# Performance work log

Hardware: AMD Instinct MI355X
Metric: run time of the kernel (lower is better)

## Reference

```python
import jax, jax.numpy as jnp
import numpy as np

NUM_HEADS = 8


def setup_inputs() -> dict:
    key = jax.random.key(0)
    ks = jax.random.split(key, 8)
    B, N, H, W = 8, 1024, 32, 32
    dim = H * W  # 1024
    x1 = jax.random.normal(ks[0], (B, N, H, W), dtype=jnp.float32)
    x2 = jax.random.normal(ks[1], (B, N, H, W), dtype=jnp.float32)
    conv_w = jax.random.normal(ks[2], (N, 2 * N, 3, 3), dtype=jnp.float32) * 0.01
    conv_b = jnp.zeros((N,), dtype=jnp.float32)
    wq = jax.random.normal(ks[3], (dim, dim), dtype=jnp.float32) * 0.02
    wk = jax.random.normal(ks[4], (dim, dim), dtype=jnp.float32) * 0.02
    wv = jax.random.normal(ks[5], (dim, dim), dtype=jnp.float32) * 0.02
    proj_w = jax.random.normal(ks[6], (dim, dim), dtype=jnp.float32) * 0.02
    proj_b = jnp.zeros((dim,), dtype=jnp.float32)
    return {"x1": x1, "x2": x2, "conv_w": conv_w, "conv_b": conv_b,
            "wq": wq, "wk": wk, "wv": wv, "proj_w": proj_w, "proj_b": proj_b}


def reference(x1, x2, conv_w, conv_b, wq, wk, wv, proj_w, proj_b):
    B, N, H, W = x1.shape
    C = H * W
    nh = NUM_HEADS
    hd = C // nh
    scale = hd ** -0.5

    # conv_cat: Conv2d(2N -> N, k=3, pad=1) on channel-concatenated inputs
    x_cat = jnp.concatenate([x1, x2], axis=1)  # [B, 2N, H, W]
    x_cat = jax.lax.conv_general_dilated(
        x_cat, conv_w, window_strides=(1, 1), padding=((1, 1), (1, 1)),
        dimension_numbers=("NCHW", "OIHW", "NCHW"))
    x_cat = x_cat + conv_b[None, :, None, None]
    x_cat = x_cat.reshape(B, N, C)  # [B, N, C]

    # torch Linear: y = x @ W.T (no bias, qkv_bias=False)
    def heads(t):  # [B, N, C] -> [B, nh, N, hd]
        return t.reshape(B, N, nh, hd).transpose(0, 2, 1, 3)

    q = heads(x1.reshape(B, N, C) @ wq.T)
    k = heads(x_cat @ wk.T)
    v = heads(x_cat @ wv.T)

    # attention: softmax(q k^T * scale) v   (dropout is identity at p=0)
    attn = jnp.einsum("bhnd,bhmd->bhnm", q, k) * scale
    attn = jax.nn.softmax(attn, axis=-1)
    x_attn = jnp.einsum("bhnm,bhmd->bhnd", attn, v)  # [B, nh, N, hd]
    x_attn = x_attn.transpose(0, 2, 1, 3).reshape(B, N, C)

    out = (x_attn @ proj_w.T + proj_b).reshape(B, N, H, W) + x1
    return out
```

## Files before the change

kernel.cpp:

```cpp
#include <hip/hip_runtime.h>
#include <hip/hip_bf16.h>
#include <cstdint>
#include <cstddef>

typedef __attribute__((ext_vector_type(8))) short short8;
typedef __attribute__((ext_vector_type(4))) float f32x4;
typedef unsigned short u16;

static __device__ __forceinline__ u16 f2bf(float f) {
  __hip_bfloat16 h = __float2bfloat16(f);
  return *reinterpret_cast<u16*>(&h);
}

static __device__ __forceinline__ void gload16(const void* g, void* l) {
  __builtin_amdgcn_global_load_lds(
      (const __attribute__((address_space(1))) void*)g,
      (__attribute__((address_space(3))) void*)l, 16, 0, 0);
}


__global__ void cast4_k(const float* __restrict__ a, const float* __restrict__ b,
                        const float* __restrict__ c, const float* __restrict__ d,
                        u16* __restrict__ oa, u16* __restrict__ ob,
                        u16* __restrict__ oc, u16* __restrict__ od) {
  const int which = blockIdx.y;
  const float* src = (which == 0) ? a : (which == 1) ? b : (which == 2) ? c : d;
  u16* dst = (which == 0) ? oa : (which == 1) ? ob : (which == 2) ? oc : od;
  int i = blockIdx.x * 256 + threadIdx.x;
  float4 v = ((const float4*)src)[i];
  union { u16 u[4]; uint2 p; } r;
  r.u[0] = f2bf(v.x); r.u[1] = f2bf(v.y); r.u[2] = f2bf(v.z); r.u[3] = f2bf(v.w);
  ((uint2*)dst)[i] = r.p;
}

__global__ void build_pad(const float* __restrict__ x1, const float* __restrict__ x2,
                          u16* __restrict__ in_t_pad, u16* __restrict__ x1b) {
  __shared__ float tile[64][65];
  const int it = blockIdx.x;
  const int st = blockIdx.y;
  const int b  = blockIdx.z;
  const int i0 = it * 64, s0 = st * 64;
  const bool isx1 = (i0 < 1024);
  const float* src = isx1
      ? x1 + ((size_t)b * 1024 + i0) * 1024
      : x2 + ((size_t)b * 1024 + (i0 - 1024)) * 1024;
  const int t = threadIdx.x;
  #pragma unroll
  for (int jj = 0; jj < 16; ++jj) {
    int idx = jj * 256 + t;
    int ii = idx >> 6, si = idx & 63;
    float v = src[(size_t)ii * 1024 + s0 + si];
    tile[ii][si] = v;
    if (isx1)
      x1b[((size_t)b * 1024 + i0 + ii) * 1024 + s0 + si] = f2bf(v);
  }
  __syncthreads();
  #pragma unroll
  for (int jj = 0; jj < 16; ++jj) {
    int idx = jj * 256 + t;
    int si = idx >> 6, ii = idx & 63;
    const int s = s0 + si;
    const int prow = (b * 34 + (s >> 5) + 1) * 34 + (s & 31) + 1;
    in_t_pad[(size_t)prow * 2048 + i0 + ii] = f2bf(tile[ii][si]);
  }
}

__global__ void pack_wp(const float* __restrict__ cw, u16* __restrict__ Wp) {
  __shared__ float sb[2304];
  const int blk = blockIdx.x;
  const int t = threadIdx.x;
  const size_t base = (size_t)blk * 2304;
  #pragma unroll
  for (int jj = 0; jj < 9; ++jj) sb[jj * 256 + t] = cw[base + jj * 256 + t];
  __syncthreads();
  const int p = blk * 256 + t;
  #pragma unroll
  for (int q = 0; q < 9; ++q)
    Wp[(size_t)q * 2097152 + p] = f2bf(sb[t * 9 + q]);
}

__global__ void addc_k(const float* __restrict__ p, const float* __restrict__ bias,
                       u16* __restrict__ xc) {
  __shared__ float tile[64][65];
  const int st = blockIdx.x;
  const int ot = blockIdx.y;
  const int b  = blockIdx.z;
  const int s0 = st * 64, o0 = ot * 64;
  const int t = threadIdx.x;
  const float* p1 = p + 8388608;
  #pragma unroll
  for (int jj = 0; jj < 16; ++jj) {
    int idx = jj * 256 + t;
    int si = idx >> 6, oi = idx & 63;
    const size_t m = ((size_t)b * 1024 + s0 + si) * 1024 + o0 + oi;
    tile[si][oi] = p[m] + p1[m] + bias[o0 + oi];
  }
  __syncthreads();
  #pragma unroll
  for (int jj = 0; jj < 16; ++jj) {
    int idx = jj * 256 + t;
    int oi = idx >> 6, si = idx & 63;
    xc[((size_t)b * 1024 + o0 + oi) * 1024 + s0 + si] = f2bf(tile[si][oi]);
  }
}

enum { GM_PLAIN = 0, GM_PROJ = 2, GM_KV = 4 };

__global__ __launch_bounds__(256, 1)
void conv9_k(const u16* __restrict__ Ap, const u16* __restrict__ B,
             float* __restrict__ Cf) {
  __shared__ u16 lds[2 * 12288 + 3 * 8192];
  const int tid = threadIdx.x;
  const int lane = tid & 63, w = tid >> 6;
  const int l15 = lane & 15, l4 = lane >> 4;

  const int bid = blockIdx.x;
  const int lb = (bid & 7) * 32 + (bid >> 3);
  const int kz = lb >> 7;
  const int tile = lb & 127;
  const int tm = tile >> 2, tn = tile & 3;
  const int row0 = tm * 256, col0 = tn * 256;
  const int b = tm >> 2;
  const int y0 = (tm & 3) * 8;
  const int hb = (b * 34 + y0) * 34;
  const int wr = (w >> 1) * 128, wc = (w & 1) * 128;
  const int chbase = kz * 1024;

  int pr[8];
  #pragma unroll
  for (int mi = 0; mi < 8; ++mi) {
    const int m = row0 + wr + mi * 16 + l15;
    const int y = (m >> 5) & 31, x = m & 31;
    pr[mi] = (y - y0 + 1) * 34 + x + 1;
  }

  const int srow = tid >> 2;
  const int sgc = tid & 3;

  f32x4 acc[8][8];
  #pragma unroll
  for (int i = 0; i < 8; ++i)
    #pragma unroll
    for (int jj = 0; jj < 8; ++jj)
      acc[i][jj] = (f32x4){0.f, 0.f, 0.f, 0.f};

  auto stageHalo = [&](int cc, int half) {
    u16* dst = lds + half * 12288;
    #pragma unroll
    for (int rnd = 0; rnd < 6; ++rnd) {
      const int row = rnd * 64 + srow;
      const int g = sgc ^ ((row >> 1) & 3);
      const u16* src = Ap + (size_t)(hb + row) * 2048 + chbase + cc * 32 + g * 8;
      gload16(src, dst + (size_t)(rnd * 256 + tid) * 8);
    }
  };
  auto stageB = [&](int cc, int q) {
    u16* dst = lds + 24576 + (q % 3) * 8192;
    #pragma unroll
    for (int rnd = 0; rnd < 4; ++rnd) {
      const int r = rnd * 64 + srow;
      const int g = sgc ^ ((r >> 1) & 3);
      const u16* src = B + ((size_t)q << 21) + (size_t)(col0 + r) * 2048
                       + chbase + cc * 32 + g * 8;
      gload16(src, dst + (size_t)(rnd * 256 + tid) * 8);
    }
  };

  constexpr int ddt[9] = {-35, -34, -33, -1, 0, 1, 33, 34, 35};
  constexpr int NC = 32;

  stageHalo(0, 0);
  stageHalo(1, 1);
  stageB(0, 0);
  stageB(0, 1);

  for (int cc = 0; cc < NC; ++cc) {
    const u16* hcur = lds + (cc & 1) * 12288;
    const bool interior = (cc >= 1 && cc <= NC - 2);
    #pragma unroll
    for (int q = 0; q < 9; ++q) {
      if ((q == 1 || q == 2) && interior) {
        asm volatile("s_waitcnt vmcnt(10)" ::: "memory");
      } else if (q == 8 && cc == NC - 1) {
        asm volatile("s_waitcnt vmcnt(0)" ::: "memory");
      } else {
        asm volatile("s_waitcnt vmcnt(4)" ::: "memory");
      }
      __builtin_amdgcn_s_barrier();
      {
        const int gp2 = cc * 9 + q + 2;
        if (gp2 <= NC * 9 - 1) {
          int qS = q + 2, ccS = cc;
          if (qS >= 9) { qS -= 9; ccS += 1; }
          stageB(ccS, qS);
        }
        if (q == 0 && cc >= 1 && cc <= NC - 2)
          stageHalo(cc + 1, (cc + 1) & 1);
      }
      {
        const u16* bq = lds + 24576 + (q % 3) * 8192;
        const int dd = ddt[q];
        short8 av[8], bv[8];
        #pragma unroll
        for (int mi = 0; mi < 8; ++mi) {
          const int hr = pr[mi] + dd;
          const int g = l4 ^ ((hr >> 1) & 3);
          av[mi] = *(const short8*)(hcur + hr * 32 + g * 8);
        }
        #pragma unroll
        for (int ni = 0; ni < 8; ++ni) {
          const int r = wc + ni * 16 + l15;
          const int g = l4 ^ ((r >> 1) & 3);
          bv[ni] = *(const short8*)(bq + r * 32 + g * 8);
        }
        __builtin_amdgcn_s_setprio(1);
        #pragma unroll
        for (int mi = 0; mi < 8; ++mi)
          #pragma unroll
          for (int ni = 0; ni < 8; ++ni)
            acc[mi][ni] = __builtin_amdgcn_mfma_f32_16x16x32_bf16(av[mi], bv[ni], acc[mi][ni], 0, 0, 0);
        __builtin_amdgcn_s_setprio(0);
      }
    }
  }

  #pragma unroll
  for (int mi = 0; mi < 8; ++mi) {
    #pragma unroll
    for (int ni = 0; ni < 8; ++ni) {
      #pragma unroll
      for (int j = 0; j < 4; ++j) {
        const int grow = row0 + wr + mi * 16 + l4 * 4 + j;
        const int gcol = col0 + wc + ni * 16 + l15;
        Cf[(size_t)kz * 8388608 + ((size_t)grow << 10) + gcol] = acc[mi][ni][j];
      }
    }
  }
}

template<int MODE>
__global__ __launch_bounds__(512, 2)
void gemm3_k(const u16* __restrict__ A, const u16* __restrict__ B,
             u16* __restrict__ Cb, float* __restrict__ Cf,
             const float* __restrict__ bias, const float* __restrict__ resid,
             int Ktot, int ntn_sh) {
  __shared__ u16 lds[3 * 24576];
  const int tid = threadIdx.x;
  const int lane = tid & 63;
  const int w = tid >> 6;
  const int l15 = lane & 15, l4 = lane >> 4;

  const int nwg = gridDim.x;
  const int bid = blockIdx.x;
  const int lb = (bid & 7) * (nwg >> 3) + (bid >> 3);
  const int tm = lb >> ntn_sh;
  const int tn = lb & ((1 << ntn_sh) - 1);
  const int row0 = tm * 256, col0 = tn * 128;
  const int wr = (w >> 1) * 64, wc = (w & 1) * 64;

  const int sr = w * 8 + (lane >> 3);
  const int pp = (lane & 7) ^ (lane >> 3);

  f32x4 acc[4][4];
  #pragma unroll
  for (int i = 0; i < 4; ++i)
    #pragma unroll
    for (int jj = 0; jj < 4; ++jj)
      acc[i][jj] = (f32x4){0.f, 0.f, 0.f, 0.f};

  const int nK = Ktot >> 6;

  auto stage = [&](int kt, u16* buf) {
    u16* da = buf + (size_t)w * 512;
    u16* db = buf + 16384 + (size_t)w * 512;
    const int k0 = kt << 6;
    #pragma unroll
    for (int u = 0; u < 4; ++u) {
      const u16* ga = A + (size_t)(row0 + u * 64 + sr) * Ktot + k0 + pp * 8;
      gload16(ga, da + u * 4096);
    }
    #pragma unroll
    for (int u = 0; u < 2; ++u) {
      const u16* gb = B + (size_t)(col0 + u * 64 + sr) * Ktot + k0 + pp * 8;
      gload16(gb, db + u * 4096);
    }
  };

  auto compute = [&](const u16* buf) {
    const char* Ar = (const char*)buf;
    const char* Br = (const char*)(buf + 16384);
    #pragma unroll
    for (int ks = 0; ks < 2; ++ks) {
      const int bcol = ((ks << 6) + (l4 << 4)) ^ ((l15 & 7) << 4);
      short8 av[4], bv[4];
      #pragma unroll
      for (int mi = 0; mi < 4; ++mi)
        av[mi] = *(const short8*)(Ar + (wr + mi * 16 + l15) * 128 + bcol);
      #pragma unroll
      for (int ni = 0; ni < 4; ++ni)
        bv[ni] = *(const short8*)(Br + (wc + ni * 16 + l15) * 128 + bcol);
      __builtin_amdgcn_s_setprio(1);
      #pragma unroll
      for (int mi = 0; mi < 4; ++mi)
        #pragma unroll
        for (int ni = 0; ni < 4; ++ni)
          acc[mi][ni] = __builtin_amdgcn_mfma_f32_16x16x32_bf16(av[mi], bv[ni], acc[mi][ni], 0, 0, 0);
      __builtin_amdgcn_s_setprio(0);
    }
  };

  u16* pb0 = lds;
  u16* pb1 = lds + 24576;
  u16* pb2 = lds + 49152;

  stage(0, pb0);
  stage(1, pb1);
  for (int t = 0; t < nK; ++t) {
    if (t + 1 < nK) {
      asm volatile("s_waitcnt vmcnt(6)" ::: "memory");
    } else {
      asm volatile("s_waitcnt vmcnt(0)" ::: "memory");
    }
    __builtin_amdgcn_s_barrier();
    if (t + 2 < nK) stage(t + 2, pb2);
    compute(pb0);
    u16* tmp = pb0; pb0 = pb1; pb1 = pb2; pb2 = tmp;
  }

  #pragma unroll
  for (int mi = 0; mi < 4; ++mi) {
    #pragma unroll
    for (int ni = 0; ni < 4; ++ni) {
      #pragma unroll
      for (int j = 0; j < 4; ++j) {
        const int grow = row0 + wr + mi * 16 + l4 * 4 + j;
        const int gcol = col0 + wc + ni * 16 + l15;
        const float v = acc[mi][ni][j];
        if constexpr (MODE == GM_PLAIN) {
          Cb[((size_t)grow << 10) + gcol] = f2bf(v);
        } else if constexpr (MODE == GM_PROJ) {
          const size_t o = ((size_t)grow << 10) + gcol;
          Cf[o] = v + bias[gcol] + resid[o];
        }
      }
    }
  }
}

template<int MODE>
__global__ __launch_bounds__(512, 4)
void gemm5_k(const u16* __restrict__ A, const u16* __restrict__ B,
             u16* __restrict__ Cb, u16* __restrict__ Cb2,
             int Ktot, int ntn_sh) {
  __shared__ u16 lds[3 * 12288];
  const int tid = threadIdx.x;
  const int lane = tid & 63;
  const int w = tid >> 6;
  const int l15 = lane & 15, l4 = lane >> 4;

  const int nwg = gridDim.x;
  const int bid = blockIdx.x;
  const int lb = (bid & 7) * (nwg >> 3) + (bid >> 3);
  const int tm = lb >> ntn_sh;
  const int tn = lb & ((1 << ntn_sh) - 1);
  const int row0 = tm * 256, col0 = tn * 128;
  const int wr = (w >> 1) * 64, wc = (w & 1) * 64;

  const int str = tid >> 2;
  const int sgc = tid & 3;

  f32x4 acc[4][4];
  #pragma unroll
  for (int i = 0; i < 4; ++i)
    #pragma unroll
    for (int jj = 0; jj < 4; ++jj)
      acc[i][jj] = (f32x4){0.f, 0.f, 0.f, 0.f};

  const int nKt = Ktot >> 5;

  auto stage = [&](int kt, u16* buf) {
    const int k0 = kt << 5;
    #pragma unroll
    for (int u = 0; u < 2; ++u) {
      const int r = u * 128 + str;
      const int swz = sgc ^ ((r >> 1) & 3);
      const u16* ga = A + (size_t)(row0 + r) * Ktot + k0 + swz * 8;
      gload16(ga, buf + ((size_t)u * 512 + tid) * 8);
    }
    {
      const int swz = sgc ^ ((str >> 1) & 3);
      const u16* gb = B + (size_t)(col0 + str) * Ktot + k0 + swz * 8;
      gload16(gb, buf + 8192 + (size_t)tid * 8);
    }
  };

  auto compute = [&](const u16* buf) {
    short8 av[4], bv[4];
    #pragma unroll
    for (int mi = 0; mi < 4; ++mi) {
      const int row = wr + mi * 16 + l15;
      const int g = l4 ^ ((row >> 1) & 3);
      av[mi] = *(const short8*)(buf + row * 32 + g * 8);
    }
    #pragma unroll
    for (int ni = 0; ni < 4; ++ni) {
      const int row = wc + ni * 16 + l15;
      const int g = l4 ^ ((row >> 1) & 3);
      bv[ni] = *(const short8*)(buf + 8192 + row * 32 + g * 8);
    }
    __builtin_amdgcn_s_setprio(1);
    #pragma unroll
    for (int mi = 0; mi < 4; ++mi)
      #pragma unroll
      for (int ni = 0; ni < 4; ++ni)
        acc[mi][ni] = __builtin_amdgcn_mfma_f32_16x16x32_bf16(av[mi], bv[ni], acc[mi][ni], 0, 0, 0);
    __builtin_amdgcn_s_setprio(0);
  };

  u16* pb0 = lds;
  u16* pb1 = lds + 12288;
  u16* pb2 = lds + 24576;

  stage(0, pb0);
  stage(1, pb1);
  for (int t = 0; t < nKt; ++t) {
    if (t + 1 < nKt) {
      asm volatile("s_waitcnt vmcnt(3)" ::: "memory");
    } else {
      asm volatile("s_waitcnt vmcnt(0)" ::: "memory");
    }
    __builtin_amdgcn_s_barrier();
    if (t + 2 < nKt) stage(t + 2, pb2);
    compute(pb0);
    u16* tmp = pb0; pb0 = pb1; pb1 = pb2; pb2 = tmp;
  }

  if constexpr (MODE == GM_KV) {
    if (col0 < 1024) {
      #pragma unroll
      for (int mi = 0; mi < 4; ++mi)
        #pragma unroll
        for (int ni = 0; ni < 4; ++ni)
          #pragma unroll
          for (int j = 0; j < 4; ++j) {
            const int grow = row0 + wr + mi * 16 + l4 * 4 + j;
            const int gcol = col0 + wc + ni * 16 + l15;
            Cb[((size_t)grow << 10) + gcol] = f2bf(acc[mi][ni][j]);
          }
    } else {
      const int h = (col0 - 1024) >> 7;
      const int bb = row0 >> 10;
      u16* tb = lds;
      #pragma unroll
      for (int chunk = 0; chunk < 4; ++chunk) {
        __syncthreads();
        if ((w >> 1) == chunk) {
          #pragma unroll
          for (int mi = 0; mi < 4; ++mi)
            #pragma unroll
            for (int ni = 0; ni < 4; ++ni)
              #pragma unroll
              for (int j = 0; j < 4; ++j) {
                const int d = wc + ni * 16 + l15;
                const int t = mi * 16 + l4 * 4 + j;
                tb[d * 66 + t] = f2bf(acc[mi][ni][j]);
              }
        }
        __syncthreads();
        {
          const int r = tid >> 2;
          const int c0 = (tid & 3) * 16;
          const int tok = (row0 & 1023) + chunk * 64 + c0;
          uint4 v0 = *(const uint4*)(tb + r * 66 + c0);
          uint4 v1 = *(const uint4*)(tb + r * 66 + c0 + 8);
          u16* dst = Cb2 + (((size_t)((bb * 8 + h) * 128 + r)) << 10) + tok;
          *(uint4*)dst = v0;
          *(uint4*)(dst + 8) = v1;
        }
      }
    }
  }
}

__global__ __launch_bounds__(256, 2)
void attn2_k(const u16* __restrict__ Q, const u16* __restrict__ K,
             const u16* __restrict__ Vt, u16* __restrict__ O) {
  __shared__ u16 Ks[2][64 * 128];
  __shared__ u16 Vs[2][128 * 64];
  __shared__ u16 Plds[4][16 * 80];
  const int bid = blockIdx.x;
  const int lb = (bid & 7) * 128 + (bid >> 3);
  const int bh = lb >> 4;
  const int mtile = lb & 15;
  const int b = bh >> 3, h = bh & 7;
  const int tid = threadIdx.x, lane = tid & 63, w = tid >> 6;
  const int l15 = lane & 15, l4 = lane >> 4;

  short8 qf[4];
  {
    const int qrow = b * 1024 + mtile * 64 + w * 16 + l15;
    const u16* qb = Q + ((size_t)qrow << 10) + h * 128;
    #pragma unroll
    for (int kk = 0; kk < 4; ++kk)
      qf[kk] = *(const short8*)(qb + kk * 32 + l4 * 8);
  }

  f32x4 o[8];
  #pragma unroll
  for (int db = 0; db < 8; ++db) o[db] = (f32x4){0.f, 0.f, 0.f, 0.f};
  float mrow[4], lrow[4];
  #pragma unroll
  for (int j = 0; j < 4; ++j) { mrow[j] = -1e30f; lrow[j] = 0.f; }
  const float scale = 0.08838834764831845f;

  auto stageKV = [&](int kt, int half) {
    #pragma unroll
    for (int j = 0; j < 4; ++j) {
      const int c = (j * 4 + w) * 64 + lane;
      const int r = c >> 4;
      const int coff = (((c & 15) ^ (r & 7)) << 3);
      const u16* gp = K + ((size_t)(b * 1024 + kt * 64 + r) << 10) + h * 128 + coff;
      gload16(gp, (void*)(Ks[half] + (j * 4 + w) * 512));
    }
    #pragma unroll
    for (int j = 0; j < 4; ++j) {
      const int c = (j * 4 + w) * 64 + lane;
      const int r = c >> 3;
      const int coff = (((c & 7) ^ (r & 7)) << 3);
      const u16* gp = Vt + ((size_t)((b * 8 + h) * 128 + r) << 10) + kt * 64 + coff;
      gload16(gp, (void*)(Vs[half] + (j * 4 + w) * 512));
    }
  };

  stageKV(0, 0);
  for (int kt = 0; kt < 16; ++kt) {
    const int cur = kt & 1;
    asm volatile("s_waitcnt vmcnt(0)" ::: "memory");
    __builtin_amdgcn_s_barrier();
    if (kt + 1 < 16) stageKV(kt + 1, cur ^ 1);

    const u16* ks_ = Ks[cur];
    const u16* vs_ = Vs[cur];
    f32x4 s[4];
    #pragma unroll
    for (int cb = 0; cb < 4; ++cb) {
      s[cb] = (f32x4){0.f, 0.f, 0.f, 0.f};
      #pragma unroll
      for (int kk = 0; kk < 4; ++kk) {
        const int col = (kk * 32 + l4 * 8) ^ ((l15 & 7) << 3);
        short8 bK = *(const short8*)(ks_ + (cb * 16 + l15) * 128 + col);
        s[cb] = __builtin_amdgcn_mfma_f32_16x16x32_bf16(qf[kk], bK, s[cb], 0, 0, 0);
      }
    }
    #pragma unroll
    for (int cb = 0; cb < 4; ++cb) {
      s[cb][0] *= scale; s[cb][1] *= scale; s[cb][2] *= scale; s[cb][3] *= scale;
    }
    #pragma unroll
    for (int j = 0; j < 4; ++j) {
      float mx = fmaxf(fmaxf(s[0][j], s[1][j]), fmaxf(s[2][j], s[3][j]));
      #pragma unroll
      for (int off = 8; off >= 1; off >>= 1)
        mx = fmaxf(mx, __shfl_xor(mx, off, 64));
      const float mn = fmaxf(mrow[j], mx);
      const float fac = __expf(mrow[j] - mn);
      mrow[j] = mn;
      float rs = 0.f;
      #pragma unroll
      for (int cb = 0; cb < 4; ++cb) {
        const float p = __expf(s[cb][j] - mn);
        s[cb][j] = p;
        rs += p;
      }
      #pragma unroll
      for (int off = 8; off >= 1; off >>= 1)
        rs += __shfl_xor(rs, off, 64);
      lrow[j] = lrow[j] * fac + rs;
      #pragma unroll
      for (int db = 0; db < 8; ++db) o[db][j] *= fac;
    }
    u16* pl = Plds[w];
    #pragma unroll
    for (int cb = 0; cb < 4; ++cb)
      #pragma unroll
      for (int j = 0; j < 4; ++j)
        pl[(l4 * 4 + j) * 80 + cb * 16 + l15] = f2bf(s[cb][j]);
    asm volatile("s_waitcnt lgkmcnt(0)" ::: "memory");
    __builtin_amdgcn_sched_barrier(0);
    short8 ap[2];
    #pragma unroll
    for (int ks2 = 0; ks2 < 2; ++ks2)
      ap[ks2] = *(const short8*)(pl + l15 * 80 + ks2 * 32 + l4 * 8);
    #pragma unroll
    for (int db = 0; db < 8; ++db) {
      #pragma unroll
      for (int ks2 = 0; ks2 < 2; ++ks2) {
        const int col = (ks2 * 32 + l4 * 8) ^ ((l15 & 7) << 3);
        short8 bV = *(const short8*)(vs_ + (db * 16 + l15) * 64 + col);
        o[db] = __builtin_amdgcn_mfma_f32_16x16x32_bf16(ap[ks2], bV, o[db], 0, 0, 0);
      }
    }
  }
  #pragma unroll
  for (int db = 0; db < 8; ++db) {
    #pragma unroll
    for (int j = 0; j < 4; ++j) {
      const int grow = b * 1024 + mtile * 64 + w * 16 + l4 * 4 + j;
      const int gcol = h * 128 + db * 16 + l15;
      O[((size_t)grow << 10) + gcol] = f2bf(o[db][j] / lrow[j]);
    }
  }
}


extern "C" void kernel_launch(void* const* d_in, const int* in_sizes, int n_in,
                              void* d_out, int out_size, void* d_ws, size_t ws_size,
                              hipStream_t stream) {
  const float* x1     = (const float*)d_in[0];
  const float* x2     = (const float*)d_in[1];
  const float* conv_w = (const float*)d_in[2];
  const float* conv_b = (const float*)d_in[3];
  const float* wq     = (const float*)d_in[4];
  const float* wk     = (const float*)d_in[5];
  const float* wv     = (const float*)d_in[6];
  const float* proj_w = (const float*)d_in[7];
  const float* proj_b = (const float*)d_in[8];
  float* out = (float*)d_out;

  char* ws = (char*)d_ws;
  size_t off = 0;
  auto alloc = [&](size_t bytes) -> void* {
    void* p = ws + off;
    off += (bytes + 255) & ~(size_t)255;
    return p;
  };
  u16* x1b  = (u16*)alloc(8192ULL * 1024 * 2);
  u16* in_t_pad = (u16*)alloc((9248ULL + 96) * 2048 * 2);
  const size_t pad_bytes = 9248ULL * 2048 * 2;
  u16* Wp   = (u16*)alloc(9ULL * 2097152 * 2);
  u16* wqb  = (u16*)alloc(1048576ULL * 2);
  u16* wkb  = (u16*)alloc(1048576ULL * 2);
  u16* wvb  = (u16*)alloc(1048576ULL * 2);
  u16* pjb  = (u16*)alloc(1048576ULL * 2);
  u16* xc   = (u16*)alloc(8192ULL * 1024 * 2);
  u16* Qb   = (u16*)alloc(8192ULL * 1024 * 2);
  u16* Kb   = (u16*)alloc(8192ULL * 1024 * 2);
  u16* Vtb  = (u16*)alloc(8192ULL * 1024 * 2);
  u16* Ob   = (u16*)alloc(8192ULL * 1024 * 2);
  float* pConv = (float*)Qb;

  (void)hipMemsetAsync(in_t_pad, 0, pad_bytes + 96ULL * 2048 * 2, stream);
  cast4_k<<<dim3(1024, 4), 256, 0, stream>>>(wq, wk, wv, proj_w, wqb, wkb, wvb, pjb);
  build_pad<<<dim3(32, 16, 8), 256, 0, stream>>>(x1, x2, in_t_pad, x1b);
  pack_wp<<<8192, 256, 0, stream>>>(conv_w, Wp);

  conv9_k<<<256, 256, 0, stream>>>(in_t_pad, Wp, pConv);
  addc_k<<<dim3(16, 16, 8), 256, 0, stream>>>(pConv, conv_b, xc);
  gemm3_k<GM_PLAIN><<<256, 512, 0, stream>>>(x1b, wqb, Qb, nullptr, nullptr, nullptr, 1024, 3);
  gemm5_k<GM_KV><<<512, 512, 0, stream>>>(xc, wkb, Kb, Vtb, 1024, 4);
  attn2_k<<<1024, 256, 0, stream>>>(Qb, Kb, Vtb, Ob);
  gemm3_k<GM_PROJ><<<256, 512, 0, stream>>>(Ob, pjb, nullptr, out, proj_b, x1, 1024, 3);
}
```

Baseline: 495.5 us.

## Merge Q/K/V GEMMs into one launch, prefetch conv A fragments, tweak attention

Measured after the change: 551.8 us. +11.4%, slower.

```diff
diff --git a/kernel.cpp b/kernel.cpp
--- a/kernel.cpp
+++ b/kernel.cpp
@@ -104,11 +104,11 @@
   }
 }
 
-enum { GM_PLAIN = 0, GM_PROJ = 2, GM_KV = 4 };
+enum { GM_PLAIN = 0, GM_PROJ = 2 };
 
 __global__ __launch_bounds__(256, 1)
-void conv9_k(const u16* __restrict__ Ap, const u16* __restrict__ B,
-             float* __restrict__ Cf) {
+void conv11_k(const u16* __restrict__ Ap, const u16* __restrict__ B,
+              float* __restrict__ Cf) {
   __shared__ u16 lds[2 * 12288 + 3 * 8192];
   const int tid = threadIdx.x;
   const int lane = tid & 63, w = tid >> 6;
@@ -174,6 +174,8 @@
   stageB(0, 0);
   stageB(0, 1);
 
+  short8 avb[2][8];
+
   for (int cc = 0; cc < NC; ++cc) {
     const u16* hcur = lds + (cc & 1) * 12288;
     const bool interior = (cc >= 1 && cc <= NC - 2);
@@ -199,26 +201,35 @@
       }
       {
         const u16* bq = lds + 24576 + (q % 3) * 8192;
-        const int dd = ddt[q];
-        short8 av[8], bv[8];
-        #pragma unroll
-        for (int mi = 0; mi < 8; ++mi) {
-          const int hr = pr[mi] + dd;
-          const int g = l4 ^ ((hr >> 1) & 3);
-          av[mi] = *(const short8*)(hcur + hr * 32 + g * 8);
+        if (q == 0) {
+          #pragma unroll
+          for (int mi = 0; mi < 8; ++mi) {
+            const int hr = pr[mi] + ddt[0];
+            const int g = l4 ^ ((hr >> 1) & 3);
+            avb[0][mi] = *(const short8*)(hcur + hr * 32 + g * 8);
+          }
         }
+        short8 bv[8];
         #pragma unroll
         for (int ni = 0; ni < 8; ++ni) {
           const int r = wc + ni * 16 + l15;
           const int g = l4 ^ ((r >> 1) & 3);
           bv[ni] = *(const short8*)(bq + r * 32 + g * 8);
         }
+        if (q < 8) {
+          #pragma unroll
+          for (int mi = 0; mi < 8; ++mi) {
+            const int hr = pr[mi] + ddt[q + 1];
+            const int g = l4 ^ ((hr >> 1) & 3);
+            avb[(q + 1) & 1][mi] = *(const short8*)(hcur + hr * 32 + g * 8);
+          }
+        }
         __builtin_amdgcn_s_setprio(1);
         #pragma unroll
         for (int mi = 0; mi < 8; ++mi)
           #pragma unroll
           for (int ni = 0; ni < 8; ++ni)
-            acc[mi][ni] = __builtin_amdgcn_mfma_f32_16x16x32_bf16(av[mi], bv[ni], acc[mi][ni], 0, 0, 0);
+            acc[mi][ni] = __builtin_amdgcn_mfma_f32_16x16x32_bf16(avb[q & 1][mi], bv[ni], acc[mi][ni], 0, 0, 0);
         __builtin_amdgcn_s_setprio(0);
       }
     }
@@ -347,25 +358,28 @@
   }
 }
 
-template<int MODE>
 __global__ __launch_bounds__(512, 4)
-void gemm5_k(const u16* __restrict__ A, const u16* __restrict__ B,
-             u16* __restrict__ Cb, u16* __restrict__ Cb2,
-             int Ktot, int ntn_sh) {
+void qkv_k(const u16* __restrict__ Ax1, const u16* __restrict__ Axc,
+           const u16* __restrict__ Wq, const u16* __restrict__ Wk,
+           const u16* __restrict__ Wv,
+           u16* __restrict__ Qb, u16* __restrict__ Kb, u16* __restrict__ Vtb) {
   __shared__ u16 lds[3 * 12288];
   const int tid = threadIdx.x;
   const int lane = tid & 63;
   const int w = tid >> 6;
   const int l15 = lane & 15, l4 = lane >> 4;
 
-  const int nwg = gridDim.x;
   const int bid = blockIdx.x;
-  const int lb = (bid & 7) * (nwg >> 3) + (bid >> 3);
-  const int tm = lb >> ntn_sh;
-  const int tn = lb & ((1 << ntn_sh) - 1);
+  const int lb = (bid & 7) * 96 + (bid >> 3);
+  const int sel = lb >> 8;
+  const int sub = lb & 255;
+  const int tm = sub >> 3, tn = sub & 7;
   const int row0 = tm * 256, col0 = tn * 128;
   const int wr = (w >> 1) * 64, wc = (w & 1) * 64;
 
+  const u16* A = (sel == 0) ? Ax1 : Axc;
+  const u16* B = (sel == 0) ? Wq : (sel == 1) ? Wk : Wv;
+
   const int str = tid >> 2;
   const int sgc = tid & 3;
 
@@ -376,6 +390,7 @@
     for (int jj = 0; jj < 4; ++jj)
       acc[i][jj] = (f32x4){0.f, 0.f, 0.f, 0.f};
 
+  constexpr int Ktot = 1024;
   const int nKt = Ktot >> 5;
 
   auto stage = [&](int kt, u16* buf) {
@@ -435,48 +450,47 @@
     u16* tmp = pb0; pb0 = pb1; pb1 = pb2; pb2 = tmp;
   }
 
-  if constexpr (MODE == GM_KV) {
-    if (col0 < 1024) {
-      #pragma unroll
-      for (int mi = 0; mi < 4; ++mi)
+  if (sel < 2) {
+    u16* Cb = (sel == 0) ? Qb : Kb;
+    #pragma unroll
+    for (int mi = 0; mi < 4; ++mi)
+      #pragma unroll
+      for (int ni = 0; ni < 4; ++ni)
         #pragma unroll
-        for (int ni = 0; ni < 4; ++ni)
+        for (int j = 0; j < 4; ++j) {
+          const int grow = row0 + wr + mi * 16 + l4 * 4 + j;
+          const int gcol = col0 + wc + ni * 16 + l15;
+          Cb[((size_t)grow << 10) + gcol] = f2bf(acc[mi][ni][j]);
+        }
+  } else {
+    const int h = tn;
+    const int bb = row0 >> 10;
+    u16* tb = lds;
+    #pragma unroll
+    for (int chunk = 0; chunk < 4; ++chunk) {
+      __syncthreads();
+      if ((w >> 1) == chunk) {
+        #pragma unroll
+        for (int mi = 0; mi < 4; ++mi)
           #pragma unroll
-          for (int j = 0; j < 4; ++j) {
-            const int grow = row0 + wr + mi * 16 + l4 * 4 + j;
-            const int gcol = col0 + wc + ni * 16 + l15;
-            Cb[((size_t)grow << 10) + gcol] = f2bf(acc[mi][ni][j]);
-          }
-    } else {
-      const int h = (col0 - 1024) >> 7;
-      const int bb = row0 >> 10;
-      u16* tb = lds;
-      #pragma unroll
-      for (int chunk = 0; chunk < 4; ++chunk) {
-        __syncthreads();
-        if ((w >> 1) == chunk) {
-          #pragma unroll
-          for (int mi = 0; mi < 4; ++mi)
+          for (int ni = 0; ni < 4; ++ni)
             #pragma unroll
-            for (int ni = 0; ni < 4; ++ni)
-              #pragma unroll
-              for (int j = 0; j < 4; ++j) {
-                const int d = wc + ni * 16 + l15;
-                const int t = mi * 16 + l4 * 4 + j;
-                tb[d * 66 + t] = f2bf(acc[mi][ni][j]);
-              }
-        }
-        __syncthreads();
-        {
-          const int r = tid >> 2;
-          const int c0 = (tid & 3) * 16;
-          const int tok = (row0 & 1023) + chunk * 64 + c0;
-          uint4 v0 = *(const uint4*)(tb + r * 66 + c0);
-          uint4 v1 = *(const uint4*)(tb + r * 66 + c0 + 8);
-          u16* dst = Cb2 + (((size_t)((bb * 8 + h) * 128 + r)) << 10) + tok;
-          *(uint4*)dst = v0;
-          *(uint4*)(dst + 8) = v1;
-        }
+            for (int j = 0; j < 4; ++j) {
+              const int d = wc + ni * 16 + l15;
+              const int t = mi * 16 + l4 * 4 + j;
+              tb[d * 66 + t] = f2bf(acc[mi][ni][j]);
+            }
+      }
+      __syncthreads();
+      {
+        const int r = tid >> 2;
+        const int c0 = (tid & 3) * 16;
+        const int tok = (row0 & 1023) + chunk * 64 + c0;
+        uint4 v0 = *(const uint4*)(tb + r * 66 + c0);
+        uint4 v1 = *(const uint4*)(tb + r * 66 + c0 + 8);
+        u16* dst = Vtb + (((size_t)((bb * 8 + h) * 128 + r)) << 10) + tok;
+        *(uint4*)dst = v0;
+        *(uint4*)(dst + 8) = v1;
       }
     }
   }
@@ -487,7 +501,7 @@
              const u16* __restrict__ Vt, u16* __restrict__ O) {
   __shared__ u16 Ks[2][64 * 128];
   __shared__ u16 Vs[2][128 * 64];
-  __shared__ u16 Plds[4][16 * 80];
+  __shared__ u16 Plds[4][16 * 72];
   const int bid = blockIdx.x;
   const int lb = (bid & 7) * 128 + (bid >> 3);
   const int bh = lb >> 4;
@@ -549,7 +563,9 @@
       for (int kk = 0; kk < 4; ++kk) {
         const int col = (kk * 32 + l4 * 8) ^ ((l15 & 7) << 3);
         short8 bK = *(const short8*)(ks_ + (cb * 16 + l15) * 128 + col);
+        __builtin_amdgcn_s_setprio(1);
         s[cb] = __builtin_amdgcn_mfma_f32_16x16x32_bf16(qf[kk], bK, s[cb], 0, 0, 0);
+        __builtin_amdgcn_s_setprio(0);
       }
     }
     #pragma unroll
@@ -584,20 +600,22 @@
     for (int cb = 0; cb < 4; ++cb)
       #pragma unroll
       for (int j = 0; j < 4; ++j)
-        pl[(l4 * 4 + j) * 80 + cb * 16 + l15] = f2bf(s[cb][j]);
+        pl[(l4 * 4 + j) * 72 + cb * 16 + l15] = f2bf(s[cb][j]);
     asm volatile("s_waitcnt lgkmcnt(0)" ::: "memory");
     __builtin_amdgcn_sched_barrier(0);
     short8 ap[2];
     #pragma unroll
     for (int ks2 = 0; ks2 < 2; ++ks2)
-      ap[ks2] = *(const short8*)(pl + l15 * 80 + ks2 * 32 + l4 * 8);
+      ap[ks2] = *(const short8*)(pl + l15 * 72 + ks2 * 32 + l4 * 8);
     #pragma unroll
     for (int db = 0; db < 8; ++db) {
       #pragma unroll
       for (int ks2 = 0; ks2 < 2; ++ks2) {
         const int col = (ks2 * 32 + l4 * 8) ^ ((l15 & 7) << 3);
         short8 bV = *(const short8*)(vs_ + (db * 16 + l15) * 64 + col);
+        __builtin_amdgcn_s_setprio(1);
         o[db] = __builtin_amdgcn_mfma_f32_16x16x32_bf16(ap[ks2], bV, o[db], 0, 0, 0);
+        __builtin_amdgcn_s_setprio(0);
       }
     }
   }
@@ -654,10 +672,9 @@
   build_pad<<<dim3(32, 16, 8), 256, 0, stream>>>(x1, x2, in_t_pad, x1b);
   pack_wp<<<8192, 256, 0, stream>>>(conv_w, Wp);
 
-  conv9_k<<<256, 256, 0, stream>>>(in_t_pad, Wp, pConv);
+  conv11_k<<<256, 256, 0, stream>>>(in_t_pad, Wp, pConv);
   addc_k<<<dim3(16, 16, 8), 256, 0, stream>>>(pConv, conv_b, xc);
-  gemm3_k<GM_PLAIN><<<256, 512, 0, stream>>>(x1b, wqb, Qb, nullptr, nullptr, nullptr, 1024, 3);
-  gemm5_k<GM_KV><<<512, 512, 0, stream>>>(xc, wkb, Kb, Vtb, 1024, 4);
+  qkv_k<<<768, 512, 0, stream>>>(x1b, xc, wqb, wkb, wvb, Qb, Kb, Vtb);
   attn2_k<<<1024, 256, 0, stream>>>(Qb, Kb, Vtb, Ob);
   gemm3_k<GM_PROJ><<<256, 512, 0, stream>>>(Ob, pjb, nullptr, out, proj_b, x1, 1024, 3);
 }
```
